# Kernel optimization log

Hardware: AMD Instinct MI355X
Metric: run time of the kernel (lower is better)

The kernel has to match this reference:

```python
import jax, jax.numpy as jnp
import numpy as np


def setup_inputs() -> dict:
    key = jax.random.key(0)
    ks = jax.random.split(key, 8)
    B, C, H, W = 8, 512, 64, 64
    Co = C // 8
    s = 0.02  # weight init scale
    return {
        'x': jax.random.normal(ks[0], (B, C, H, W), jnp.float32),
        'Wq': jax.random.normal(ks[1], (Co, C), jnp.float32) * s,
        'bq': jnp.zeros((Co,), jnp.float32),
        'Wk': jax.random.normal(ks[2], (Co, C), jnp.float32) * s,
        'bk': jnp.zeros((Co,), jnp.float32),
        'Wv': jax.random.normal(ks[3], (C, C), jnp.float32) * s,
        'bv': jnp.zeros((C,), jnp.float32),
        'gamma': jax.random.normal(ks[4], (1,), jnp.float32) * 0.1,
    }


def reference(x, Wq, bq, Wk, bk, Wv, bv, gamma):
    B, C, H, W = x.shape
    # 1x1 convs == channel contractions
    q = jnp.einsum('oc,bchw->bohw', Wq, x) + bq[None, :, None, None]
    k = jnp.einsum('oc,bchw->bohw', Wk, x) + bk[None, :, None, None]
    v = jnp.einsum('oc,bchw->bohw', Wv, x) + bv[None, :, None, None]
    # column (H-axis) energies, diagonal masked to -inf to avoid double count
    eH = jnp.einsum('bohw,boiw->bhwi', q, k)  # [B,H,W,H2]
    diag_mask = jnp.where(jnp.eye(H, dtype=bool), -jnp.inf, 0.0)  # [H,H2]
    eH = eH + diag_mask[None, :, None, :]
    # row (W-axis) energies
    eW = jnp.einsum('bohw,bohj->bhwj', q, k)  # [B,H,W,W2]
    # joint softmax over concatenated H+W axis
    attn = jax.nn.softmax(jnp.concatenate([eH, eW], axis=-1), axis=-1)
    aH, aW = attn[..., :H], attn[..., H:]
    out = jnp.einsum('bciw,bhwi->bchw', v, aH) + jnp.einsum('bchj,bhwj->bchw', v, aW)
    return gamma[0] * out + x
```

## Files before the change

kernel.cpp:

```cpp
#include <hip/hip_runtime.h>
#include <hip/hip_bf16.h>

#define NB 8
#define NC 512
#define NO 64
#define NH 64
#define NW 64
#define NHW 4096

typedef __attribute__((ext_vector_type(8))) short bf16x8;
typedef __attribute__((ext_vector_type(4))) float f32x4;

__device__ __forceinline__ void gload16(const void* g, void* l) {
    __builtin_amdgcn_global_load_lds(
        (const __attribute__((address_space(1))) void*)g,
        (__attribute__((address_space(3))) void*)l, 16, 0, 0);
}

__device__ __forceinline__ short f2bf_bits(float f) {
    __hip_bfloat16 h = __float2bfloat16(f);
    short s; __builtin_memcpy(&s, &h, 2); return s;
}
__device__ __forceinline__ float bfbits_to_f(short s) {
    unsigned int u = ((unsigned int)(unsigned short)s) << 16;
    float f; __builtin_memcpy(&f, &u, 4); return f;
}

__global__ __launch_bounds__(256) void pack_w(
    const float* __restrict__ Wq, const float* __restrict__ bq,
    const float* __restrict__ Wk, const float* __restrict__ bk,
    const float* __restrict__ Wv, const float* __restrict__ bv,
    __hip_bfloat16* __restrict__ Wbf, float* __restrict__ bias_all)
{
    const int row = blockIdx.x;
    const int t = threadIdx.x;
    const float* src; float bias;
    if (row < 64)       { src = Wq + row*NC;        bias = bq[row]; }
    else if (row < 128) { src = Wk + (row-64)*NC;   bias = bk[row-64]; }
    else                { src = Wv + (row-128)*NC;  bias = bv[row-128]; }
    for (int i = t; i < NC; i += 256)
        Wbf[(size_t)row*NC + i] = __float2bfloat16(src[i]);
    if (t == 0) bias_all[row] = bias;
}

__global__ __launch_bounds__(256) void transpose_x(
    const float* __restrict__ x, __hip_bfloat16* __restrict__ xt)
{
    __shared__ float tile[64][65];
    const int c0  = blockIdx.x * 64;
    const int hw0 = blockIdx.y * 64;
    const int b   = blockIdx.z;
    const int t = threadIdx.x;
    const int col = t & 63, r4 = t >> 6;
    #pragma unroll
    for (int s = 0; s < 16; ++s) {
        int cr = s*4 + r4;
        tile[cr][col] = x[((size_t)b*NC + c0 + cr)*NHW + hw0 + col];
    }
    __syncthreads();
    #pragma unroll
    for (int s = 0; s < 16; ++s) {
        int wr = s*4 + r4;
        xt[((size_t)b*NHW + hw0 + wr)*NC + c0 + col] = __float2bfloat16(tile[col][wr]);
    }
}

__global__ __launch_bounds__(256) void qkv_mfma(
    const __hip_bfloat16* __restrict__ xt, const __hip_bfloat16* __restrict__ Wbf,
    const float* __restrict__ bias_all,
    __hip_bfloat16* __restrict__ qkT2, __hip_bfloat16* __restrict__ vb)
{
    __shared__ __align__(16) char As[2][16384];
    __shared__ __align__(16) char Bs[2][16384];
    const int t = threadIdx.x;
    const int lane = t & 63;
    const int wv = t >> 6;
    const int wm = wv >> 1, wn = wv & 1;
    const int fr = lane & 15, fg = lane >> 4;
    const int hw0 = blockIdx.x * 128;
    const int y   = blockIdx.y;
    const int b   = blockIdx.z;
    const int o0s = (y == 4) ? 0 : (128 + y*128);
    const __hip_bfloat16* xtb = xt + (size_t)b * NHW * NC;

#define STAGE(ksrc, buf)                                                    \
    {                                                                       \
        _Pragma("unroll")                                                   \
        for (int s = 0; s < 4; ++s) {                                       \
            int linear = s*256 + t;                                         \
            int row = linear >> 3, g = linear & 7;                          \
            int gk = (g ^ (row & 7)) * 8;                                   \
            gload16(Wbf + (size_t)(o0s + row)*NC + (ksrc)*64 + gk,          \
                    As[buf] + linear*16);                                   \
            gload16(xtb + (size_t)(hw0 + row)*NC + (ksrc)*64 + gk,          \
                    Bs[buf] + linear*16);                                   \
        }                                                                   \
    }

    STAGE(0, 0);
    __syncthreads();

    f32x4 acc[4][4] = {};

    for (int ks = 0; ks < 8; ++ks) {
        const int cur = ks & 1, nxt = cur ^ 1;
        if (ks < 7) STAGE(ks+1, nxt);
        const char* Ms = (y == 4) ? Bs[cur] : As[cur];
        const char* Ns = (y == 4) ? As[cur] : Bs[cur];
        #pragma unroll
        for (int kk = 0; kk < 2; ++kk) {
            const int gl = kk*4 + fg;
            bf16x8 m1[4], n1[4];
            #pragma unroll
            for (int mf = 0; mf < 4; ++mf) {
                int r = wm*64 + mf*16 + fr;
                m1[mf] = *(const bf16x8*)(Ms + r*128 + ((gl ^ (r & 7)) << 4));
            }
            #pragma unroll
            for (int nf = 0; nf < 4; ++nf) {
                int c = wn*64 + nf*16 + fr;
                n1[nf] = *(const bf16x8*)(Ns + c*128 + ((gl ^ (c & 7)) << 4));
            }
            #pragma unroll
            for (int mf = 0; mf < 4; ++mf)
                #pragma unroll
                for (int nf = 0; nf < 4; ++nf)
                    acc[mf][nf] = __builtin_amdgcn_mfma_f32_16x16x32_bf16(
                        m1[mf], n1[nf], acc[mf][nf], 0, 0, 0);
        }
        if (ks < 7) __syncthreads();
    }
#undef STAGE

    if (y < 4) {
        #pragma unroll
        for (int mf = 0; mf < 4; ++mf) {
            #pragma unroll
            for (int reg = 0; reg < 4; ++reg) {
                int o = o0s + wm*64 + mf*16 + (lane >> 4)*4 + reg;
                float bias = bias_all[o];
                size_t rowbase = ((size_t)b*NC + (o - 128))*NHW;
                #pragma unroll
                for (int nf = 0; nf < 4; ++nf) {
                    int hw = hw0 + wn*64 + nf*16 + (lane & 15);
                    vb[rowbase + hw] = __float2bfloat16(acc[mf][nf][reg] + bias);
                }
            }
        }
    } else {
        #pragma unroll
        for (int mf = 0; mf < 4; ++mf) {
            #pragma unroll
            for (int reg = 0; reg < 4; ++reg) {
                int hwl = wm*64 + mf*16 + (lane >> 4)*4 + reg;
                size_t rbase = ((size_t)b*NHW + hw0 + hwl)*128;
                #pragma unroll
                for (int nf = 0; nf < 4; ++nf) {
                    int col = wn*64 + nf*16 + (lane & 15);
                    qkT2[rbase + col] = __float2bfloat16(acc[mf][nf][reg] + bias_all[col]);
                }
            }
        }
    }
}

__global__ __launch_bounds__(256) void transpose_hw(
    const __hip_bfloat16* __restrict__ src_, __hip_bfloat16* __restrict__ dst_,
    int nch)
{
    __shared__ __align__(16) short tile[4][64*64];
    const int t = threadIdx.x, wv = t >> 6, lane = t & 63;
    const int c = blockIdx.x*4 + wv, b = blockIdx.y;
    const __hip_bfloat16* src = src_ + ((size_t)(b*nch + c))*NHW;
    __hip_bfloat16* dst = dst_ + ((size_t)(b*nch + c))*NHW;
    short* tl = tile[wv];
    #pragma unroll
    for (int s = 0; s < 8; ++s) {
        int i = s*8 + (lane>>3), w0 = (lane&7)*8;
        bf16x8 vv = *(const bf16x8*)(src + i*64 + w0);
        *(bf16x8*)&tl[i*64 + (((w0>>3) ^ ((i>>3)&7)) << 3)] = vv;
    }
    __syncthreads();
    #pragma unroll
    for (int s = 0; s < 8; ++s) {
        int w = s*8 + (lane>>3), i0 = (lane&7)*8;
        bf16x8 ov;
        #pragma unroll
        for (int d = 0; d < 8; ++d)
            ov[d] = tl[(i0+d)*64 + (((w>>3) ^ (lane&7)) << 3) + (w&7)];
        *(bf16x8*)(dst + w*64 + i0) = ov;
    }
}

__global__ __launch_bounds__(256) void scores_mfma(
    const __hip_bfloat16* __restrict__ qkT2,
    __hip_bfloat16* __restrict__ rawH, __hip_bfloat16* __restrict__ rawW)
{
    __shared__ __align__(16) char Qs[64*128];
    __shared__ __align__(16) char Ks[64*128];
    const int t = threadIdx.x, lane = t & 63, wv = t >> 6;
    const int wm = wv >> 1, wn = wv & 1;
    const int fr = lane & 15, fg = lane >> 4;
    const int s = blockIdx.x, y = blockIdx.y, b = blockIdx.z;
    const __hip_bfloat16* base = qkT2 + (size_t)b * NHW * 128;
    #pragma unroll
    for (int i = 0; i < 2; ++i) {
        int linear = i*256 + t;
        int r = linear >> 3, g = linear & 7;
        int gk = (g ^ (r & 7)) * 8;
        size_t ro = (y == 0) ? ((size_t)(r*64 + s) * 128)
                             : ((size_t)(s*64 + r) * 128);
        gload16(base + ro + gk,      Qs + linear*16);
        gload16(base + ro + 64 + gk, Ks + linear*16);
    }
    __syncthreads();
    f32x4 acc[2][2] = {};
    #pragma unroll
    for (int kk = 0; kk < 2; ++kk) {
        const int gl = kk*4 + fg;
        bf16x8 qf[2], kf[2];
        #pragma unroll
        for (int mf = 0; mf < 2; ++mf) {
            int r = wm*32 + mf*16 + fr;
            qf[mf] = *(const bf16x8*)(Qs + r*128 + ((gl ^ (r & 7)) << 4));
        }
        #pragma unroll
        for (int nf = 0; nf < 2; ++nf) {
            int c = wn*32 + nf*16 + fr;
            kf[nf] = *(const bf16x8*)(Ks + c*128 + ((gl ^ (c & 7)) << 4));
        }
        #pragma unroll
        for (int mf = 0; mf < 2; ++mf)
            #pragma unroll
            for (int nf = 0; nf < 2; ++nf)
                acc[mf][nf] = __builtin_amdgcn_mfma_f32_16x16x32_bf16(
                    qf[mf], kf[nf], acc[mf][nf], 0, 0, 0);
    }
    __hip_bfloat16* dst = (y == 0) ? rawH : rawW;
    const size_t dbase = ((size_t)(b*64 + s)) * 4096;
    #pragma unroll
    for (int mf = 0; mf < 2; ++mf) {
        #pragma unroll
        for (int reg = 0; reg < 4; ++reg) {
            int row = wm*32 + mf*16 + (lane >> 4)*4 + reg;
            #pragma unroll
            for (int nf = 0; nf < 2; ++nf) {
                int col = wn*32 + nf*16 + (lane & 15);
                dst[dbase + (size_t)row*64 + col] = __float2bfloat16(acc[mf][nf][reg]);
            }
        }
    }
}

__global__ __launch_bounds__(256) void softmax_ab(
    const __hip_bfloat16* __restrict__ rawH, const __hip_bfloat16* __restrict__ rawW,
    __hip_bfloat16* __restrict__ aHb, __hip_bfloat16* __restrict__ aWb)
{
    __shared__ float sH[64][65];
    __shared__ float sW[64][65];
    __shared__ float red[8][64];
    const int t = threadIdx.x;
    const int w = t & 63, p = t >> 6;
    const int hb = blockIdx.x, b = blockIdx.y;
    #pragma unroll
    for (int i2 = 0; i2 < 2; ++i2) {
        int linear = i2*256 + t;
        int ww = linear >> 3, g = linear & 7;
        bf16x8 hv = *(const bf16x8*)(rawH + (((size_t)(b*64 + ww))*64 + hb)*64 + g*8);
        bf16x8 wvv = *(const bf16x8*)(rawW + (((size_t)(b*64 + hb))*64 + ww)*64 + g*8);
        #pragma unroll
        for (int e = 0; e < 8; ++e) {
            sH[ww][g*8+e] = bfbits_to_f(hv[e]);
            sW[ww][g*8+e] = bfbits_to_f(wvv[e]);
        }
    }
    __syncthreads();
    if (t < 64) sH[t][hb] = -1e30f;
    __syncthreads();
    float m = -1e30f;
    #pragma unroll
    for (int z = 0; z < 32; ++z) {
        float val = (p < 2) ? sH[w][p*32+z] : sW[w][(p-2)*32+z];
        m = fmaxf(m, val);
    }
    red[p][w] = m;
    __syncthreads();
    float M = fmaxf(fmaxf(red[0][w], red[1][w]), fmaxf(red[2][w], red[3][w]));
    float ssum = 0.f;
    #pragma unroll
    for (int z = 0; z < 32; ++z) {
        float* slot = (p < 2) ? &sH[w][p*32+z] : &sW[w][(p-2)*32+z];
        float e = __expf(*slot - M);
        ssum += e;
        *slot = e;
    }
    red[4+p][w] = ssum;
    __syncthreads();
    float S = red[4][w] + red[5][w] + red[6][w] + red[7][w];
    float rinv = 1.f / S;
    if (p < 2) {
        size_t base = (((size_t)b*NH + w)*NH + hb)*NO + p*32;
        #pragma unroll
        for (int zz = 0; zz < 4; ++zz) {
            bf16x8 pk;
            #pragma unroll
            for (int d = 0; d < 8; ++d)
                pk[d] = f2bf_bits(sH[w][p*32 + zz*8 + d] * rinv);
            *(bf16x8*)(aHb + base + zz*8) = pk;
        }
    } else {
        size_t base = (((size_t)b*NH + hb)*NH + w)*NO + (p-2)*32;
        #pragma unroll
        for (int zz = 0; zz < 4; ++zz) {
            bf16x8 pk;
            #pragma unroll
            for (int d = 0; d < 8; ++d)
                pk[d] = f2bf_bits(sW[w][(p-2)*32 + zz*8 + d] * rinv);
            *(bf16x8*)(aWb + base + zz*8) = pk;
        }
    }
}

__global__ __launch_bounds__(256) void col_mfma(
    const __hip_bfloat16* __restrict__ vT, const __hip_bfloat16* __restrict__ aH,
    __hip_bfloat16* __restrict__ PT)
{
    __shared__ __align__(16) char As[64*128];
    __shared__ __align__(16) char Bs[256*128];
    const int t = threadIdx.x, lane = t & 63, wn = t >> 6;
    const int fr = lane & 15, fg = lane >> 4;
    const int w = blockIdx.x, chalf = blockIdx.y, b = blockIdx.z;
    const __hip_bfloat16* Ag = aH + ((size_t)(b*NH + w))*4096;
    const __hip_bfloat16* Bg = vT + ((size_t)(b*NC + chalf*256))*NHW + w*64;
    #pragma unroll
    for (int s = 0; s < 2; ++s) {
        int linear = s*256 + t;
        int r = linear >> 3, g = linear & 7;
        gload16(Ag + r*64 + ((g ^ (r&7)) * 8), As + linear*16);
    }
    #pragma unroll
    for (int s = 0; s < 8; ++s) {
        int linear = s*256 + t;
        int r = linear >> 3, g = linear & 7;
        gload16(Bg + (size_t)r*NHW + ((g ^ (r&7)) * 8), Bs + linear*16);
    }
    __syncthreads();
    f32x4 acc[4][4] = {};
    #pragma unroll
    for (int kk = 0; kk < 2; ++kk) {
        int gl = kk*4 + fg;
        bf16x8 af[4], bfv[4];
        #pragma unroll
        for (int mf = 0; mf < 4; ++mf) {
            int r = mf*16 + fr;
            af[mf] = *(const bf16x8*)(As + r*128 + ((gl ^ (r&7)) << 4));
        }
        #pragma unroll
        for (int nf = 0; nf < 4; ++nf) {
            int c = wn*64 + nf*16 + fr;
            bfv[nf] = *(const bf16x8*)(Bs + c*128 + ((gl ^ (c&7)) << 4));
        }
        #pragma unroll
        for (int mf = 0; mf < 4; ++mf)
            #pragma unroll
            for (int nf = 0; nf < 4; ++nf)
                acc[mf][nf] = __builtin_amdgcn_mfma_f32_16x16x32_bf16(
                    af[mf], bfv[nf], acc[mf][nf], 0, 0, 0);
    }
    const size_t base = ((size_t)(b*NH + w))*64*512 + chalf*256;
    #pragma unroll
    for (int mf = 0; mf < 4; ++mf) {
        #pragma unroll
        for (int reg = 0; reg < 4; ++reg) {
            int hh = mf*16 + (lane >> 4)*4 + reg;
            #pragma unroll
            for (int nf = 0; nf < 4; ++nf) {
                int cc = wn*64 + nf*16 + (lane & 15);
                PT[base + (size_t)hh*512 + cc] = __float2bfloat16(acc[mf][nf][reg]);
            }
        }
    }
}

__global__ __launch_bounds__(256) void row_mfma(
    const __hip_bfloat16* __restrict__ vb, const __hip_bfloat16* __restrict__ aW,
    const __hip_bfloat16* __restrict__ PT, const float* __restrict__ x,
    const float* __restrict__ gamma, float* __restrict__ out)
{
    __shared__ __align__(16) char Ws[64*128];
    __shared__ __align__(16) char Vs[128*128];
    __shared__ __align__(16) short PTs[64*136];
    const int t = threadIdx.x, lane = t & 63, wm = t >> 6;
    const int fr = lane & 15, fg = lane >> 4;
    const int h = blockIdx.x, cq = blockIdx.y, b = blockIdx.z;
    const int c0 = cq*128;
    const __hip_bfloat16* Ag = aW + ((size_t)(b*NH + h))*4096;
    const __hip_bfloat16* Vg = vb + ((size_t)(b*NC + c0))*NHW + h*64;
    #pragma unroll
    for (int s = 0; s < 2; ++s) {
        int linear = s*256 + t;
        int r = linear >> 3, g = linear & 7;
        gload16(Ag + r*64 + ((g ^ (r&7)) * 8), Ws + linear*16);
    }
    #pragma unroll
    for (int s = 0; s < 4; ++s) {
        int linear = s*256 + t;
        int r = linear >> 3, g = linear & 7;
        gload16(Vg + (size_t)r*NHW + ((g ^ (r&7)) * 8), Vs + linear*16);
    }
    #pragma unroll
    for (int s = 0; s < 4; ++s) {
        int idx = s*256 + t;
        int ww = idx >> 4, cg = idx & 15;
        bf16x8 pv = *(const bf16x8*)(PT + (((size_t)(b*NH + ww))*64 + h)*512 + c0 + cg*8);
        *(bf16x8*)&PTs[ww*136 + cg*8] = pv;
    }
    __syncthreads();
    f32x4 acc[2][4] = {};
    #pragma unroll
    for (int kk = 0; kk < 2; ++kk) {
        int gl = kk*4 + fg;
        bf16x8 vf[2], wf[4];
        #pragma unroll
        for (int mf = 0; mf < 2; ++mf) {
            int c = wm*32 + mf*16 + fr;
            vf[mf] = *(const bf16x8*)(Vs + c*128 + ((gl ^ (c&7)) << 4));
        }
        #pragma unroll
        for (int nf = 0; nf < 4; ++nf) {
            int ww = nf*16 + fr;
            wf[nf] = *(const bf16x8*)(Ws + ww*128 + ((gl ^ (ww&7)) << 4));
        }
        #pragma unroll
        for (int mf = 0; mf < 2; ++mf)
            #pragma unroll
            for (int nf = 0; nf < 4; ++nf)
                acc[mf][nf] = __builtin_amdgcn_mfma_f32_16x16x32_bf16(
                    vf[mf], wf[nf], acc[mf][nf], 0, 0, 0);
    }
    const float g = gamma[0];
    #pragma unroll
    for (int mf = 0; mf < 2; ++mf) {
        #pragma unroll
        for (int reg = 0; reg < 4; ++reg) {
            int cl = wm*32 + mf*16 + (lane >> 4)*4 + reg;
            size_t rowbase = ((size_t)(b*NC + c0 + cl)*NH + h)*NW;
            #pragma unroll
            for (int nf = 0; nf < 4; ++nf) {
                int ww = nf*16 + (lane & 15);
                float ptv = bfbits_to_f(PTs[ww*136 + cl]);
                out[rowbase + ww] = g*(acc[mf][nf][reg] + ptv) + x[rowbase + ww];
            }
        }
    }
}

extern "C" void kernel_launch(void* const* d_in, const int* in_sizes, int n_in,
                              void* d_out, int out_size, void* d_ws, size_t ws_size,
                              hipStream_t stream) {
    (void)in_sizes; (void)n_in; (void)out_size; (void)ws_size;
    const float* x     = (const float*)d_in[0];
    const float* Wq    = (const float*)d_in[1];
    const float* bq    = (const float*)d_in[2];
    const float* Wk    = (const float*)d_in[3];
    const float* bk    = (const float*)d_in[4];
    const float* Wv    = (const float*)d_in[5];
    const float* bv    = (const float*)d_in[6];
    const float* gamma = (const float*)d_in[7];
    float* out = (float*)d_out;

    char* p = (char*)d_ws;
    __hip_bfloat16* Wbf  = (__hip_bfloat16*)(p);
    float* bias_all      = (float*)(p + 655360);
    __hip_bfloat16* qkT2 = (__hip_bfloat16*)(p + 657920);
    __hip_bfloat16* vb   = (__hip_bfloat16*)(p + 9046528);
    __hip_bfloat16* xt   = (__hip_bfloat16*)(p + 42600960);
    __hip_bfloat16* vT   = (__hip_bfloat16*)(p + 42600960);
    __hip_bfloat16* aHb  = (__hip_bfloat16*)(p + 76155392);
    __hip_bfloat16* aWb  = (__hip_bfloat16*)(p + 80349696);
    __hip_bfloat16* PT   = (__hip_bfloat16*)(p + 84544000);
    __hip_bfloat16* rawH = PT;
    __hip_bfloat16* rawW = (__hip_bfloat16*)(p + 84544000 + 8388608);

    pack_w<<<dim3(640), 256, 0, stream>>>(Wq, bq, Wk, bk, Wv, bv, Wbf, bias_all);
    transpose_x<<<dim3(8, 64, NB), 256, 0, stream>>>(x, xt);
    qkv_mfma<<<dim3(32, 5, NB), 256, 0, stream>>>(xt, Wbf, bias_all, qkT2, vb);
    transpose_hw<<<dim3(128, NB), 256, 0, stream>>>(vb, vT, NC);
    scores_mfma<<<dim3(64, 2, NB), 256, 0, stream>>>(qkT2, rawH, rawW);
    softmax_ab<<<dim3(NH, NB), 256, 0, stream>>>(rawH, rawW, aHb, aWb);
    col_mfma<<<dim3(NW, 2, NB), 256, 0, stream>>>(vT, aHb, PT);
    row_mfma<<<dim3(NH, 4, NB), 256, 0, stream>>>(vb, aWb, PT, x, gamma, out);
}
```

Measured before the change: 121.9 us.

## Keep full x tile resident in LDS and loop over all output tiles per block

The QKV projection kernel now loads the whole 128x512 bf16 x tile into LDS once and iterates over all five output-channel tiles inside one block, streaming only the weight tiles with double buffering. The goal is to stop re-reading the same x tile from global memory five times. In exchange the grid shrinks from 1280 to 256 blocks, and the large LDS footprint (about 160KB) limits each CU to one block, which reduces occupancy and parallelism.

```diff
diff --git a/kernel.cpp b/kernel.cpp
--- a/kernel.cpp
+++ b/kernel.cpp
@@ -65,103 +65,124 @@
     }
 }
 
-__global__ __launch_bounds__(256) void qkv_mfma(
+__global__ __launch_bounds__(256) void qkv_mega(
     const __hip_bfloat16* __restrict__ xt, const __hip_bfloat16* __restrict__ Wbf,
     const float* __restrict__ bias_all,
     __hip_bfloat16* __restrict__ qkT2, __hip_bfloat16* __restrict__ vb)
 {
     __shared__ __align__(16) char As[2][16384];
-    __shared__ __align__(16) char Bs[2][16384];
+    __shared__ __align__(16) char Bs[131072];
     const int t = threadIdx.x;
     const int lane = t & 63;
     const int wv = t >> 6;
     const int wm = wv >> 1, wn = wv & 1;
     const int fr = lane & 15, fg = lane >> 4;
     const int hw0 = blockIdx.x * 128;
-    const int y   = blockIdx.y;
-    const int b   = blockIdx.z;
-    const int o0s = (y == 4) ? 0 : (128 + y*128);
+    const int b   = blockIdx.y;
     const __hip_bfloat16* xtb = xt + (size_t)b * NHW * NC;
 
-#define STAGE(ksrc, buf)                                                    \
+#define STAGE_A(o0s, ksrc, buf)                                             \
     {                                                                       \
         _Pragma("unroll")                                                   \
         for (int s = 0; s < 4; ++s) {                                       \
             int linear = s*256 + t;                                         \
             int row = linear >> 3, g = linear & 7;                          \
             int gk = (g ^ (row & 7)) * 8;                                   \
-            gload16(Wbf + (size_t)(o0s + row)*NC + (ksrc)*64 + gk,          \
+            gload16(Wbf + (size_t)((o0s) + row)*NC + (ksrc)*64 + gk,        \
                     As[buf] + linear*16);                                   \
-            gload16(xtb + (size_t)(hw0 + row)*NC + (ksrc)*64 + gk,          \
-                    Bs[buf] + linear*16);                                   \
         }                                                                   \
     }
 
-    STAGE(0, 0);
-    __syncthreads();
-
-    f32x4 acc[4][4] = {};
-
-    for (int ks = 0; ks < 8; ++ks) {
-        const int cur = ks & 1, nxt = cur ^ 1;
-        if (ks < 7) STAGE(ks+1, nxt);
-        const char* Ms = (y == 4) ? Bs[cur] : As[cur];
-        const char* Ns = (y == 4) ? As[cur] : Bs[cur];
-        #pragma unroll
-        for (int kk = 0; kk < 2; ++kk) {
-            const int gl = kk*4 + fg;
-            bf16x8 m1[4], n1[4];
+    #pragma unroll
+    for (int it = 0; it < 32; ++it) {
+        int linear = it*256 + t;
+        int row = linear >> 6, g = linear & 63;
+        int sg = (g & 56) | ((g & 7) ^ (row & 7));
+        gload16(xtb + (size_t)(hw0 + row)*NC + sg*8, Bs + linear*16);
+    }
+    STAGE_A(128, 0, 0);
+    __syncthreads();
+
+    int cur = 0;
+    for (int ot = 0; ot < 5; ++ot) {
+        const bool qk = (ot == 4);
+        const int o0s = qk ? 0 : (128 + ot*128);
+        f32x4 acc[4][4] = {};
+        for (int ks = 0; ks < 8; ++ks) {
+            const int nxt = cur ^ 1;
+            if (ks < 7)      STAGE_A(o0s, ks+1, nxt)
+            else if (ot < 4) STAGE_A((ot == 3) ? 0 : (128 + (ot+1)*128), 0, nxt)
+
+            #pragma unroll
+            for (int kk = 0; kk < 2; ++kk) {
+                const int gl = kk*4 + fg;
+                bf16x8 m1[4], n1[4];
+                if (!qk) {
+                    #pragma unroll
+                    for (int mf = 0; mf < 4; ++mf) {
+                        int r = wm*64 + mf*16 + fr;
+                        m1[mf] = *(const bf16x8*)(As[cur] + r*128 + ((gl ^ (r & 7)) << 4));
+                    }
+                    #pragma unroll
+                    for (int nf = 0; nf < 4; ++nf) {
+                        int c = wn*64 + nf*16 + fr;
+                        n1[nf] = *(const bf16x8*)(Bs + c*1024 + ((ks*8 + (gl ^ (c & 7))) << 4));
+                    }
+                } else {
+                    #pragma unroll
+                    for (int mf = 0; mf < 4; ++mf) {
+                        int r = wm*64 + mf*16 + fr;
+                        m1[mf] = *(const bf16x8*)(Bs + r*1024 + ((ks*8 + (gl ^ (r & 7))) << 4));
+                    }
+                    #pragma unroll
+                    for (int nf = 0; nf < 4; ++nf) {
+                        int c = wn*64 + nf*16 + fr;
+                        n1[nf] = *(const bf16x8*)(As[cur] + c*128 + ((gl ^ (c & 7)) << 4));
+                    }
+                }
+                #pragma unroll
+                for (int mf = 0; mf < 4; ++mf)
+                    #pragma unroll
+                    for (int nf = 0; nf < 4; ++nf)
+                        acc[mf][nf] = __builtin_amdgcn_mfma_f32_16x16x32_bf16(
+                            m1[mf], n1[nf], acc[mf][nf], 0, 0, 0);
+            }
+            __syncthreads();
+            cur ^= 1;
+        }
+
+        if (!qk) {
             #pragma unroll
             for (int mf = 0; mf < 4; ++mf) {
-                int r = wm*64 + mf*16 + fr;
-                m1[mf] = *(const bf16x8*)(Ms + r*128 + ((gl ^ (r & 7)) << 4));
-            }
-            #pragma unroll
-            for (int nf = 0; nf < 4; ++nf) {
-                int c = wn*64 + nf*16 + fr;
-                n1[nf] = *(const bf16x8*)(Ns + c*128 + ((gl ^ (c & 7)) << 4));
-            }
-            #pragma unroll
-            for (int mf = 0; mf < 4; ++mf)
                 #pragma unroll
-                for (int nf = 0; nf < 4; ++nf)
-                    acc[mf][nf] = __builtin_amdgcn_mfma_f32_16x16x32_bf16(
-                        m1[mf], n1[nf], acc[mf][nf], 0, 0, 0);
-        }
-        if (ks < 7) __syncthreads();
-    }
-#undef STAGE
-
-    if (y < 4) {
-        #pragma unroll
-        for (int mf = 0; mf < 4; ++mf) {
-            #pragma unroll
-            for (int reg = 0; reg < 4; ++reg) {
-                int o = o0s + wm*64 + mf*16 + (lane >> 4)*4 + reg;
-                float bias = bias_all[o];
-                size_t rowbase = ((size_t)b*NC + (o - 128))*NHW;
-                #pragma unroll
-                for (int nf = 0; nf < 4; ++nf) {
-                    int hw = hw0 + wn*64 + nf*16 + (lane & 15);
-                    vb[rowbase + hw] = __float2bfloat16(acc[mf][nf][reg] + bias);
+                for (int reg = 0; reg < 4; ++reg) {
+                    int o = o0s + wm*64 + mf*16 + (lane >> 4)*4 + reg;
+                    float bias = bias_all[o];
+                    size_t rowbase = ((size_t)b*NC + (o - 128))*NHW;
+                    #pragma unroll
+                    for (int nf = 0; nf < 4; ++nf) {
+                        int hw = hw0 + wn*64 + nf*16 + (lane & 15);
+                        vb[rowbase + hw] = __float2bfloat16(acc[mf][nf][reg] + bias);
+                    }
                 }
             }
-        }
-    } else {
-        #pragma unroll
-        for (int mf = 0; mf < 4; ++mf) {
-            #pragma unroll
-            for (int reg = 0; reg < 4; ++reg) {
-                int hwl = wm*64 + mf*16 + (lane >> 4)*4 + reg;
-                size_t rbase = ((size_t)b*NHW + hw0 + hwl)*128;
+        } else {
+            #pragma unroll
+            for (int mf = 0; mf < 4; ++mf) {
                 #pragma unroll
-                for (int nf = 0; nf < 4; ++nf) {
-                    int col = wn*64 + nf*16 + (lane & 15);
-                    qkT2[rbase + col] = __float2bfloat16(acc[mf][nf][reg] + bias_all[col]);
+                for (int reg = 0; reg < 4; ++reg) {
+                    int hwl = wm*64 + mf*16 + (lane >> 4)*4 + reg;
+                    size_t rbase = ((size_t)b*NHW + hw0 + hwl)*128;
+                    #pragma unroll
+                    for (int nf = 0; nf < 4; ++nf) {
+                        int col = wn*64 + nf*16 + (lane & 15);
+                        qkT2[rbase + col] = __float2bfloat16(acc[mf][nf][reg] + bias_all[col]);
+                    }
                 }
             }
         }
     }
+#undef STAGE_A
 }
 
 __global__ __launch_bounds__(256) void transpose_hw(
@@ -484,7 +505,7 @@
 
     pack_w<<<dim3(640), 256, 0, stream>>>(Wq, bq, Wk, bk, Wv, bv, Wbf, bias_all);
     transpose_x<<<dim3(8, 64, NB), 256, 0, stream>>>(x, xt);
-    qkv_mfma<<<dim3(32, 5, NB), 256, 0, stream>>>(xt, Wbf, bias_all, qkT2, vb);
+    qkv_mega<<<dim3(32, NB), 256, 0, stream>>>(xt, Wbf, bias_all, qkT2, vb);
     transpose_hw<<<dim3(128, NB), 256, 0, stream>>>(vb, vT, NC);
     scores_mfma<<<dim3(64, 2, NB), 256, 0, stream>>>(qkT2, rawH, rawW);
     softmax_ab<<<dim3(NH, NB), 256, 0, stream>>>(rawH, rawW, aHb, aWb);
```

Result: slower. 133.9 us (+9.9%).

## Fuse x transpose and bf16 cast into QKV projection GEMM loads

Applied to the files above, without the earlier changes.

Removes the separate transpose_x kernel and its bf16 xt intermediate. The QKV GEMM now reads fp32 x directly in channel-major order, converts it to bf16 in registers, and writes it transposed into swizzled LDS, with register prefetch of the next k-slice. This saves a full read/write pass over x plus one kernel launch. In exchange, x (fp32) is re-read by each of the 5 y-blocks instead of a half-size bf16 copy, and the GEMM main loop gains more VGPR pressure and conversion work.

```diff
diff --git a/kernel.cpp b/kernel.cpp
--- a/kernel.cpp
+++ b/kernel.cpp
@@ -43,30 +43,8 @@
     if (t == 0) bias_all[row] = bias;
 }
 
-__global__ __launch_bounds__(256) void transpose_x(
-    const float* __restrict__ x, __hip_bfloat16* __restrict__ xt)
-{
-    __shared__ float tile[64][65];
-    const int c0  = blockIdx.x * 64;
-    const int hw0 = blockIdx.y * 64;
-    const int b   = blockIdx.z;
-    const int t = threadIdx.x;
-    const int col = t & 63, r4 = t >> 6;
-    #pragma unroll
-    for (int s = 0; s < 16; ++s) {
-        int cr = s*4 + r4;
-        tile[cr][col] = x[((size_t)b*NC + c0 + cr)*NHW + hw0 + col];
-    }
-    __syncthreads();
-    #pragma unroll
-    for (int s = 0; s < 16; ++s) {
-        int wr = s*4 + r4;
-        xt[((size_t)b*NHW + hw0 + wr)*NC + c0 + col] = __float2bfloat16(tile[col][wr]);
-    }
-}
-
-__global__ __launch_bounds__(256) void qkv_mfma(
-    const __hip_bfloat16* __restrict__ xt, const __hip_bfloat16* __restrict__ Wbf,
+__global__ __launch_bounds__(256) void qkv_fused(
+    const float* __restrict__ x, const __hip_bfloat16* __restrict__ Wbf,
     const float* __restrict__ bias_all,
     __hip_bfloat16* __restrict__ qkT2, __hip_bfloat16* __restrict__ vb)
 {
@@ -81,9 +59,12 @@
     const int y   = blockIdx.y;
     const int b   = blockIdx.z;
     const int o0s = (y == 4) ? 0 : (128 + y*128);
-    const __hip_bfloat16* xtb = xt + (size_t)b * NHW * NC;
-
-#define STAGE(ksrc, buf)                                                    \
+    const float* xb = x + (size_t)b*NC*NHW + hw0;
+    const int oct = t >> 5, hwg = t & 31;
+
+    float4 xr[8];
+
+#define STAGE_A(ksrc, buf)                                                  \
     {                                                                       \
         _Pragma("unroll")                                                   \
         for (int s = 0; s < 4; ++s) {                                       \
@@ -92,19 +73,38 @@
             int gk = (g ^ (row & 7)) * 8;                                   \
             gload16(Wbf + (size_t)(o0s + row)*NC + (ksrc)*64 + gk,          \
                     As[buf] + linear*16);                                   \
-            gload16(xtb + (size_t)(hw0 + row)*NC + (ksrc)*64 + gk,          \
-                    Bs[buf] + linear*16);                                   \
         }                                                                   \
     }
-
-    STAGE(0, 0);
+#define LOAD_B(ksrc)                                                        \
+    {                                                                       \
+        const float* gp = xb + (size_t)((ksrc)*64 + oct*8)*NHW + hwg*4;     \
+        _Pragma("unroll")                                                   \
+        for (int e = 0; e < 8; ++e)                                         \
+            xr[e] = *(const float4*)(gp + (size_t)e*NHW);                   \
+    }
+#define WRITE_B(buf)                                                        \
+    {                                                                       \
+        _Pragma("unroll")                                                   \
+        for (int d = 0; d < 4; ++d) {                                       \
+            int row = hwg*4 + d;                                            \
+            bf16x8 wv8;                                                     \
+            _Pragma("unroll")                                               \
+            for (int e = 0; e < 8; ++e)                                     \
+                wv8[e] = f2bf_bits(((const float*)&xr[e])[d]);              \
+            *(bf16x8*)(Bs[buf] + row*128 + ((oct ^ (row & 7)) << 4)) = wv8; \
+        }                                                                   \
+    }
+
+    LOAD_B(0);
+    STAGE_A(0, 0);
+    WRITE_B(0);
     __syncthreads();
 
     f32x4 acc[4][4] = {};
 
     for (int ks = 0; ks < 8; ++ks) {
         const int cur = ks & 1, nxt = cur ^ 1;
-        if (ks < 7) STAGE(ks+1, nxt);
+        if (ks < 7) { STAGE_A(ks+1, nxt); LOAD_B(ks+1); }
         const char* Ms = (y == 4) ? Bs[cur] : As[cur];
         const char* Ns = (y == 4) ? As[cur] : Bs[cur];
         #pragma unroll
@@ -128,9 +128,14 @@
                     acc[mf][nf] = __builtin_amdgcn_mfma_f32_16x16x32_bf16(
                         m1[mf], n1[nf], acc[mf][nf], 0, 0, 0);
         }
-        if (ks < 7) __syncthreads();
-    }
-#undef STAGE
+        if (ks < 7) {
+            WRITE_B(nxt);
+            __syncthreads();
+        }
+    }
+#undef STAGE_A
+#undef LOAD_B
+#undef WRITE_B
 
     if (y < 4) {
         #pragma unroll
@@ -474,7 +479,6 @@
     float* bias_all      = (float*)(p + 655360);
     __hip_bfloat16* qkT2 = (__hip_bfloat16*)(p + 657920);
     __hip_bfloat16* vb   = (__hip_bfloat16*)(p + 9046528);
-    __hip_bfloat16* xt   = (__hip_bfloat16*)(p + 42600960);
     __hip_bfloat16* vT   = (__hip_bfloat16*)(p + 42600960);
     __hip_bfloat16* aHb  = (__hip_bfloat16*)(p + 76155392);
     __hip_bfloat16* aWb  = (__hip_bfloat16*)(p + 80349696);
@@ -483,8 +487,7 @@
     __hip_bfloat16* rawW = (__hip_bfloat16*)(p + 84544000 + 8388608);
 
     pack_w<<<dim3(640), 256, 0, stream>>>(Wq, bq, Wk, bk, Wv, bv, Wbf, bias_all);
-    transpose_x<<<dim3(8, 64, NB), 256, 0, stream>>>(x, xt);
-    qkv_mfma<<<dim3(32, 5, NB), 256, 0, stream>>>(xt, Wbf, bias_all, qkT2, vb);
+    qkv_fused<<<dim3(32, 5, NB), 256, 0, stream>>>(x, Wbf, bias_all, qkT2, vb);
     transpose_hw<<<dim3(128, NB), 256, 0, stream>>>(vb, vT, NC);
     scores_mfma<<<dim3(64, 2, NB), 256, 0, stream>>>(qkT2, rawH, rawW);
     softmax_ab<<<dim3(NH, NB), 256, 0, stream>>>(rawH, rawW, aHb, aWb);
```

Result: no change. 121.5 us (-0.3%).
